# Optimization experiments

Measured on AMD Instinct MI355X. Metric: run time of the kernel, lower is better.

The kernel has to match this reference:

```python
import jax, jax.numpy as jnp
import numpy as np
from jax import lax

BN_EPS = 1e-5

def _bn(x, g, b):
    # eval-mode BatchNorm with default running stats (mean=0, var=1)
    sh = (1, -1) + (1,) * (x.ndim - 2)
    return x * (g / jnp.sqrt(1.0 + BN_EPS)).reshape(sh) + b.reshape(sh)

def _simam(x, lam=1e-4):
    axes = tuple(range(2, x.ndim))
    mu = x.mean(axis=axes, keepdims=True)
    d2 = (x - mu) ** 2
    var = d2.mean(axis=axes, keepdims=True)
    e = d2 / (2.0 * var + 1e-12) + lam
    return jax.nn.sigmoid(1.0 / (e + 1e-12)) * x

def _dwconv1d(x, w, pad, groups):
    return lax.conv_general_dilated(
        x, w, (1,), [(pad, pad)],
        dimension_numbers=('NCH', 'OIH', 'NCH'),
        feature_group_count=groups)

def _adaptive_pool_matrix(t_in, t_out):
    # torch AdaptiveAvgPool1d: window i = [floor(i*t_in/t_out), ceil((i+1)*t_in/t_out))
    M = np.zeros((t_in, t_out), dtype=np.float32)
    for i in range(t_out):
        s = (i * t_in) // t_out
        e = -(-((i + 1) * t_in) // t_out)
        M[s:e, i] = 1.0 / (e - s)
    return jnp.asarray(M)

def _deform_conv1d(x, w, ow, ob):
    # depthwise deformable conv1d, padding='valid'; grid_sample bilinear,
    # zeros padding, align_corners=True -> pure 1D bilinear gather at pos.
    B, C, T = x.shape
    K = w.shape[1]
    T_out = T - K + 1
    off = _dwconv1d(x, ow, 0, C) + ob[None, :, None]        # (B, C*K, T_out)
    off = off.reshape(B, C, K, T_out)
    pos = (jnp.arange(T_out, dtype=x.dtype)[None, None, None, :]
           + jnp.arange(K, dtype=x.dtype)[None, None, :, None] + off)
    i0f = jnp.floor(pos)
    f = pos - i0f
    i0 = i0f.astype(jnp.int32)
    xb = jnp.broadcast_to(x[:, :, None, :], (B, C, K, T))
    def gather(idx):
        valid = (idx >= 0) & (idx < T)
        v = jnp.take_along_axis(xb, jnp.clip(idx, 0, T - 1), axis=3)
        return jnp.where(valid, v, 0.0)
    samp = gather(i0) * (1.0 - f) + gather(i0 + 1) * f      # (B,C,K,T_out)
    return jnp.einsum('bckt,ck->bct', samp, w)

def _branch(x, sw, g1, b1, tw, g2, b2):
    # spatial depthwise conv (kernel covers full channel axis) -> (B,5,T)
    h = jnp.einsum('bcht,ch->bct', x, sw)
    h = _simam(jax.nn.elu(_bn(h, g1, b1)))
    h = _dwconv1d(h, tw, tw.shape[-1] // 2, h.shape[1])     # temporal depthwise, same length
    return _simam(jax.nn.elu(_bn(h, g2, b2)))

def setup_inputs() -> dict:
    key = jax.random.key(0)
    ks = iter(jax.random.split(key, 48))
    B, C_in, T, n_class = 256, 22, 1000, 4
    k1, k2, k3 = 15, 31, 63  # _odd(round(fs*{0.06,0.12,0.25})), fs=250
    def rn(shape, scale=0.1):
        return scale * jax.random.normal(next(ks), shape, dtype=jnp.float32)
    inp = {'x': jax.random.normal(next(ks), (B, 1, C_in, T), dtype=jnp.float32),
           'stem_w': rn((15, 1, 2, 3)),
           'stem_g': 1.0 + rn((15,)), 'stem_b': rn((15,))}
    for i, kt in zip((1, 2, 3), (k1, k2, k3)):
        inp[f'b{i}_sw'] = rn((5, C_in))
        inp[f'b{i}_g1'] = 1.0 + rn((5,)); inp[f'b{i}_b1'] = rn((5,))
        inp[f'b{i}_tw'] = rn((5, 1, kt))
        inp[f'b{i}_g2'] = 1.0 + rn((5,)); inp[f'b{i}_b2'] = rn((5,))
    inp['pw_w'] = rn((5, 15))
    inp['pw_g'] = 1.0 + rn((5,)); inp['pw_b'] = rn((5,))
    inp['d1_w'] = rn((5, 5));  inp['d1_ow'] = rn((25, 1, 5), 0.02);  inp['d1_ob'] = jnp.zeros((25,), jnp.float32)
    inp['d2_w'] = rn((5, 10)); inp['d2_ow'] = rn((50, 1, 10), 0.02); inp['d2_ob'] = jnp.zeros((50,), jnp.float32)
    inp['fc_w'] = rn((n_class, 5 * 25)); inp['fc_b'] = rn((n_class,))
    return inp

def reference(x, stem_w, stem_g, stem_b,
              b1_sw, b1_g1, b1_b1, b1_tw, b1_g2, b1_b2,
              b2_sw, b2_g1, b2_b1, b2_tw, b2_g2, b2_b2,
              b3_sw, b3_g1, b3_b1, b3_tw, b3_g2, b3_b2,
              pw_w, pw_g, pw_b,
              d1_w, d1_ow, d1_ob, d2_w, d2_ow, d2_ob,
              fc_w, fc_b):
    # stem: conv2d k=(2,3) 'same' (torch pads extra on the right for even k)
    h = lax.conv_general_dilated(x, stem_w, (1, 1), [(0, 1), (1, 1)],
                                 dimension_numbers=('NCHW', 'OIHW', 'NCHW'))
    h = jax.nn.elu(_bn(h, stem_g, stem_b))                  # (B,15,22,T); dropout = eval no-op
    o1 = _branch(h[:, 0:5],  b1_sw, b1_g1, b1_b1, b1_tw, b1_g2, b1_b2)
    o2 = _branch(h[:, 5:10], b2_sw, b2_g1, b2_b1, b2_tw, b2_g2, b2_b2)
    o3 = _branch(h[:, 10:15], b3_sw, b3_g1, b3_b1, b3_tw, b3_g2, b3_b2)
    hc = jnp.concatenate([o1, o2, o3], axis=1)              # (B,15,T)
    hc = jnp.einsum('bct,to->bco', hc, _adaptive_pool_matrix(hc.shape[-1], 40))
    hc = jnp.einsum('bct,oc->bot', hc, pw_w)                # 1x1 pointwise
    hc = _simam(jax.nn.elu(_bn(hc, pw_g, pw_b)))            # (B,5,40)
    hc = _deform_conv1d(hc, d1_w, d1_ow, d1_ob)             # (B,5,36)
    hc = _deform_conv1d(hc, d2_w, d2_ow, d2_ob)             # (B,5,27)
    hc = jnp.einsum('bct,to->bco', hc, _adaptive_pool_matrix(hc.shape[-1], 25))
    return hc.reshape(hc.shape[0], -1) @ fc_w.T + fc_b      # (B,n_class)
```

## Files before the change

kernel.cpp:

```cpp
#include <hip/hip_runtime.h>
#include <math.h>

#define BNS 0.99999500003749972f

__device__ __forceinline__ float eluf(float v) {
    return v > 0.f ? v : (__expf(v) - 1.f);
}
__device__ __forceinline__ float sigmf(float u) {
    return 1.f / (1.f + __expf(-u));
}
__device__ __forceinline__ int zpw(int i) { return i + (i >> 5); }

__device__ __forceinline__ void block_reduce2(float& s1, float& s2, float* red) {
#pragma unroll
    for (int m = 32; m > 0; m >>= 1) {
        s1 += __shfl_xor(s1, m, 64);
        s2 += __shfl_xor(s2, m, 64);
    }
    const int wid = threadIdx.x >> 6, lane = threadIdx.x & 63;
    if (lane == 0) { red[wid * 2] = s1; red[wid * 2 + 1] = s2; }
    __syncthreads();
    s1 = red[0] + red[2] + red[4] + red[6];
    s2 = red[1] + red[3] + red[5] + red[7];
}

__global__ __launch_bounds__(256) void k_stem_reg(
    const float* __restrict__ x,
    const float* __restrict__ stem_w,
    const float* __restrict__ stem_g, const float* __restrict__ stem_b,
    const float* __restrict__ sw1, const float* __restrict__ sw2, const float* __restrict__ sw3,
    float* __restrict__ pre)
{
    const int tid = threadIdx.x;
    if (tid >= 250) return;
    const int b = blockIdx.z;
    const int g = blockIdx.y;
    const int t0 = (blockIdx.x * 250 + tid) * 2;
    const float* xb = x + b * 22000;

    const float* swp = (g == 0 ? sw1 : g == 1 ? sw2 : sw3);
    float w[5][6], gs[5], bs[5];
#pragma unroll
    for (int c = 0; c < 5; ++c) {
        const int C = g * 5 + c;
#pragma unroll
        for (int j = 0; j < 6; ++j) w[c][j] = stem_w[C * 6 + j];
        gs[c] = stem_g[C] * BNS;
        bs[c] = stem_b[C];
    }

    const bool sel0 = (t0 == 0), sel2 = (t0 == 998);
    const int base = sel0 ? 0 : (sel2 ? 996 : t0 - 1);

    float acc0[5] = {0, 0, 0, 0, 0}, acc1[5] = {0, 0, 0, 0, 0};

    float a0, b0, c0, d0, a1, b1, c1, d1;
    {
        const float4 v = *reinterpret_cast<const float4*>(xb + base);
        a0 = sel2 ? v.y : (sel0 ? 0.f : v.x);
        b0 = sel0 ? v.x : (sel2 ? v.z : v.y);
        c0 = sel0 ? v.y : (sel2 ? v.w : v.z);
        d0 = sel0 ? v.z : (sel2 ? 0.f : v.w);
    }
#pragma unroll
    for (int i = 0; i < 22; ++i) {
        if (i < 21) {
            const float4 v = *reinterpret_cast<const float4*>(xb + (i + 1) * 1000 + base);
            a1 = sel2 ? v.y : (sel0 ? 0.f : v.x);
            b1 = sel0 ? v.x : (sel2 ? v.z : v.y);
            c1 = sel0 ? v.y : (sel2 ? v.w : v.z);
            d1 = sel0 ? v.z : (sel2 ? 0.f : v.w);
        } else {
            a1 = b1 = c1 = d1 = 0.f;
        }
#pragma unroll
        for (int c = 0; c < 5; ++c) {
            float v0 = w[c][0] * a0 + w[c][1] * b0 + w[c][2] * c0
                     + w[c][3] * a1 + w[c][4] * b1 + w[c][5] * c1;
            float v1 = w[c][0] * b0 + w[c][1] * c0 + w[c][2] * d0
                     + w[c][3] * b1 + w[c][4] * c1 + w[c][5] * d1;
            v0 = eluf(v0 * gs[c] + bs[c]);
            v1 = eluf(v1 * gs[c] + bs[c]);
            const float sv = swp[c * 22 + i];
            acc0[c] += v0 * sv;
            acc1[c] += v1 * sv;
        }
        a0 = a1; b0 = b1; c0 = c1; d0 = d1;
    }
#pragma unroll
    for (int c = 0; c < 5; ++c) {
        float2 o; o.x = acc0[c]; o.y = acc1[c];
        *reinterpret_cast<float2*>(pre + (b * 15 + g * 5 + c) * 1000 + t0) = o;
    }
}

#define PAD 32

template<int K>
__device__ __forceinline__ void branch_body(
    const float* __restrict__ row,
    float g1s, float b1v,
    const float* __restrict__ twp,
    float g2s, float b2v,
    float* __restrict__ out40,
    float* zbuf, float* red)
{
    const int tid = threadIdx.x;
    const int t0 = tid * 4;
    const bool act = tid < 250;

    if (tid < 32) { zbuf[zpw(tid)] = 0.f; zbuf[zpw(1032 + tid)] = 0.f; }

    float y0 = 0.f, y1 = 0.f, y2 = 0.f, y3 = 0.f, s1 = 0.f, s2 = 0.f;
    if (act) {
        const float4 v = *reinterpret_cast<const float4*>(row + t0);
        y0 = eluf(v.x * g1s + b1v);
        y1 = eluf(v.y * g1s + b1v);
        y2 = eluf(v.z * g1s + b1v);
        y3 = eluf(v.w * g1s + b1v);
        s1 = y0 + y1 + y2 + y3;
        s2 = y0 * y0 + y1 * y1 + y2 * y2 + y3 * y3;
    }
    block_reduce2(s1, s2, red);
    {
        const float mu = s1 * 1e-3f;
        const float var = s2 * 1e-3f - mu * mu;
        const float iv = 1.f / (2.f * var + 1e-12f);
        if (act) {
            float d;
            d = y0 - mu; zbuf[zpw(PAD + t0 + 0)] = sigmf(1.f / (d * d * iv + 1e-4f + 1e-12f)) * y0;
            d = y1 - mu; zbuf[zpw(PAD + t0 + 1)] = sigmf(1.f / (d * d * iv + 1e-4f + 1e-12f)) * y1;
            d = y2 - mu; zbuf[zpw(PAD + t0 + 2)] = sigmf(1.f / (d * d * iv + 1e-4f + 1e-12f)) * y2;
            d = y3 - mu; zbuf[zpw(PAD + t0 + 3)] = sigmf(1.f / (d * d * iv + 1e-4f + 1e-12f)) * y3;
        }
    }
    __syncthreads();

    float u0 = 0.f, u1 = 0.f, u2 = 0.f, u3 = 0.f;
    s1 = 0.f; s2 = 0.f;
    if (act) {
        const int Lb = PAD + t0 - (K / 2);
        float q0 = zbuf[zpw(Lb + 0)];
        float q1 = zbuf[zpw(Lb + 1)];
        float q2 = zbuf[zpw(Lb + 2)];
        float q3 = zbuf[zpw(Lb + 3)];
        float a0 = 0.f, a1 = 0.f, a2 = 0.f, a3 = 0.f;
#pragma unroll
        for (int d = 0; d < K; ++d) {
            const float wv = twp[d];
            a0 += q0 * wv; a1 += q1 * wv; a2 += q2 * wv; a3 += q3 * wv;
            q0 = q1; q1 = q2; q2 = q3;
            q3 = zbuf[zpw(Lb + d + 4)];
        }
        u0 = eluf(a0 * g2s + b2v);
        u1 = eluf(a1 * g2s + b2v);
        u2 = eluf(a2 * g2s + b2v);
        u3 = eluf(a3 * g2s + b2v);
        s1 = u0 + u1 + u2 + u3;
        s2 = u0 * u0 + u1 * u1 + u2 * u2 + u3 * u3;
    }
    block_reduce2(s1, s2, red);
    {
        const float mu = s1 * 1e-3f;
        const float var = s2 * 1e-3f - mu * mu;
        const float iv = 1.f / (2.f * var + 1e-12f);
        if (act) {
            float d;
            d = u0 - mu; zbuf[zpw(PAD + t0 + 0)] = sigmf(1.f / (d * d * iv + 1e-4f + 1e-12f)) * u0;
            d = u1 - mu; zbuf[zpw(PAD + t0 + 1)] = sigmf(1.f / (d * d * iv + 1e-4f + 1e-12f)) * u1;
            d = u2 - mu; zbuf[zpw(PAD + t0 + 2)] = sigmf(1.f / (d * d * iv + 1e-4f + 1e-12f)) * u2;
            d = u3 - mu; zbuf[zpw(PAD + t0 + 3)] = sigmf(1.f / (d * d * iv + 1e-4f + 1e-12f)) * u3;
        }
    }
    __syncthreads();

    if (tid < 40) {
        float s = 0.f;
        for (int j = 0; j < 25; ++j) s += zbuf[zpw(PAD + tid * 25 + j)];
        out40[tid] = s * (1.f / 25.f);
    }
}

__global__ __launch_bounds__(256) void k_branch_row(
    const float* __restrict__ pre,
    const float* __restrict__ g1a, const float* __restrict__ b1a,
    const float* __restrict__ tw1,
    const float* __restrict__ g2a, const float* __restrict__ b2a,
    const float* __restrict__ g1b, const float* __restrict__ b1b,
    const float* __restrict__ tw2,
    const float* __restrict__ g2b, const float* __restrict__ b2b,
    const float* __restrict__ g1c, const float* __restrict__ b1c,
    const float* __restrict__ tw3,
    const float* __restrict__ g2c, const float* __restrict__ b2c,
    float* __restrict__ pooled)
{
    __shared__ float zbuf[1100];
    __shared__ float red[8];

    const int bid = blockIdx.x;
    const int b = bid / 15, C = bid % 15;
    const int br = C / 5, c = C % 5;

    const float* row = pre + (b * 15 + C) * 1000;
    float* out40 = pooled + (b * 15 + C) * 40;

    if (br == 0) {
        branch_body<15>(row, g1a[c] * BNS, b1a[c], tw1 + c * 15, g2a[c] * BNS, b2a[c], out40, zbuf, red);
    } else if (br == 1) {
        branch_body<31>(row, g1b[c] * BNS, b1b[c], tw2 + c * 31, g2b[c] * BNS, b2b[c], out40, zbuf, red);
    } else {
        branch_body<63>(row, g1c[c] * BNS, b1c[c], tw3 + c * 63, g2c[c] * BNS, b2c[c], out40, zbuf, red);
    }
}

__global__ __launch_bounds__(128) void k_head(
    const float* __restrict__ pooled,
    const float* __restrict__ pw_w, const float* __restrict__ pw_g, const float* __restrict__ pw_b,
    const float* __restrict__ d1_w, const float* __restrict__ d1_ow, const float* __restrict__ d1_ob,
    const float* __restrict__ d2_w, const float* __restrict__ d2_ow, const float* __restrict__ d2_ob,
    const float* __restrict__ fc_w, const float* __restrict__ fc_b,
    float* __restrict__ out)
{
    __shared__ float P[600];
    __shared__ float A[200];
    __shared__ float Bv[200];
    __shared__ float C1[180];
    __shared__ float C2[135];
    __shared__ float D[125];
    __shared__ float mu5[5], iv5[5];

    const int b = blockIdx.x, tid = threadIdx.x;

    for (int i = tid; i < 600; i += 128) P[i] = pooled[b * 600 + i];
    __syncthreads();

    for (int i = tid; i < 200; i += 128) {
        int o = i / 40, t = i % 40;
        float s = 0.f;
        for (int cc = 0; cc < 15; ++cc) s += P[cc * 40 + t] * pw_w[o * 15 + cc];
        float v = s * (pw_g[o] * BNS) + pw_b[o];
        A[i] = eluf(v);
    }
    __syncthreads();

    if (tid < 5) {
        float s = 0.f;
        for (int t = 0; t < 40; ++t) s += A[tid * 40 + t];
        float mu = s * (1.f / 40.f);
        float v2 = 0.f;
        for (int t = 0; t < 40; ++t) { float d = A[tid * 40 + t] - mu; v2 += d * d; }
        mu5[tid] = mu;
        iv5[tid] = 1.f / (2.f * (v2 * (1.f / 40.f)) + 1e-12f);
    }
    __syncthreads();

    for (int i = tid; i < 200; i += 128) {
        int o = i / 40;
        float a = A[i];
        float d = a - mu5[o];
        float e = d * d * iv5[o] + 1e-4f;
        Bv[i] = sigmf(1.f / (e + 1e-12f)) * a;
    }
    __syncthreads();

    for (int i = tid; i < 180; i += 128) {
        int cc = i / 36, t = i % 36;
        float o = 0.f;
        for (int k = 0; k < 5; ++k) {
            float off = d1_ob[cc * 5 + k];
            for (int d = 0; d < 5; ++d) off += Bv[cc * 40 + t + d] * d1_ow[(cc * 5 + k) * 5 + d];
            float pos = (float)(t + k) + off;
            float fl = floorf(pos);
            float f = pos - fl;
            int i0 = (int)fl;
            float v0 = (i0 >= 0 && i0 < 40) ? Bv[cc * 40 + i0] : 0.f;
            float v1 = (i0 + 1 >= 0 && i0 + 1 < 40) ? Bv[cc * 40 + i0 + 1] : 0.f;
            o += (v0 * (1.f - f) + v1 * f) * d1_w[cc * 5 + k];
        }
        C1[i] = o;
    }
    __syncthreads();

    for (int i = tid; i < 135; i += 128) {
        int cc = i / 27, t = i % 27;
        float o = 0.f;
        for (int k = 0; k < 10; ++k) {
            float off = d2_ob[cc * 10 + k];
            for (int d = 0; d < 10; ++d) off += C1[cc * 36 + t + d] * d2_ow[(cc * 10 + k) * 10 + d];
            float pos = (float)(t + k) + off;
            float fl = floorf(pos);
            float f = pos - fl;
            int i0 = (int)fl;
            float v0 = (i0 >= 0 && i0 < 36) ? C1[cc * 36 + i0] : 0.f;
            float v1 = (i0 + 1 >= 0 && i0 + 1 < 36) ? C1[cc * 36 + i0 + 1] : 0.f;
            o += (v0 * (1.f - f) + v1 * f) * d2_w[cc * 10 + k];
        }
        C2[i] = o;
    }
    __syncthreads();

    for (int i = tid; i < 125; i += 128) {
        int cc = i / 25, j = i % 25;
        int s0 = (j * 27) / 25;
        int e0 = ((j + 1) * 27 + 24) / 25;
        float s = 0.f;
        for (int q = s0; q < e0; ++q) s += C2[cc * 27 + q];
        D[i] = s / (float)(e0 - s0);
    }
    __syncthreads();

    if (tid < 64) {
        float part0 = 0.f, part1 = 0.f, part2 = 0.f, part3 = 0.f;
        for (int i = tid; i < 125; i += 64) {
            const float dv = D[i];
            part0 += dv * fc_w[0 * 125 + i];
            part1 += dv * fc_w[1 * 125 + i];
            part2 += dv * fc_w[2 * 125 + i];
            part3 += dv * fc_w[3 * 125 + i];
        }
#pragma unroll
        for (int m = 32; m > 0; m >>= 1) {
            part0 += __shfl_xor(part0, m, 64);
            part1 += __shfl_xor(part1, m, 64);
            part2 += __shfl_xor(part2, m, 64);
            part3 += __shfl_xor(part3, m, 64);
        }
        if (tid == 0) {
            out[b * 4 + 0] = part0 + fc_b[0];
            out[b * 4 + 1] = part1 + fc_b[1];
            out[b * 4 + 2] = part2 + fc_b[2];
            out[b * 4 + 3] = part3 + fc_b[3];
        }
    }
}

extern "C" void kernel_launch(void* const* d_in, const int* in_sizes, int n_in,
                              void* d_out, int out_size, void* d_ws, size_t ws_size,
                              hipStream_t stream) {
    const float* x      = (const float*)d_in[0];
    const float* stem_w = (const float*)d_in[1];
    const float* stem_g = (const float*)d_in[2];
    const float* stem_b = (const float*)d_in[3];
    const float* b1_sw = (const float*)d_in[4];
    const float* b1_g1 = (const float*)d_in[5];
    const float* b1_b1 = (const float*)d_in[6];
    const float* b1_tw = (const float*)d_in[7];
    const float* b1_g2 = (const float*)d_in[8];
    const float* b1_b2 = (const float*)d_in[9];
    const float* b2_sw = (const float*)d_in[10];
    const float* b2_g1 = (const float*)d_in[11];
    const float* b2_b1 = (const float*)d_in[12];
    const float* b2_tw = (const float*)d_in[13];
    const float* b2_g2 = (const float*)d_in[14];
    const float* b2_b2 = (const float*)d_in[15];
    const float* b3_sw = (const float*)d_in[16];
    const float* b3_g1 = (const float*)d_in[17];
    const float* b3_b1 = (const float*)d_in[18];
    const float* b3_tw = (const float*)d_in[19];
    const float* b3_g2 = (const float*)d_in[20];
    const float* b3_b2 = (const float*)d_in[21];
    const float* pw_w  = (const float*)d_in[22];
    const float* pw_g  = (const float*)d_in[23];
    const float* pw_b  = (const float*)d_in[24];
    const float* d1_w  = (const float*)d_in[25];
    const float* d1_ow = (const float*)d_in[26];
    const float* d1_ob = (const float*)d_in[27];
    const float* d2_w  = (const float*)d_in[28];
    const float* d2_ow = (const float*)d_in[29];
    const float* d2_ob = (const float*)d_in[30];
    const float* fc_w  = (const float*)d_in[31];
    const float* fc_b  = (const float*)d_in[32];

    float* pre    = (float*)d_ws;
    float* pooled = (float*)((char*)d_ws + (size_t)256 * 15 * 1000 * 4);

    k_stem_reg<<<dim3(2, 3, 256), 256, 0, stream>>>(
        x, stem_w, stem_g, stem_b, b1_sw, b2_sw, b3_sw, pre);

    k_branch_row<<<3840, 256, 0, stream>>>(
        pre,
        b1_g1, b1_b1, b1_tw, b1_g2, b1_b2,
        b2_g1, b2_b1, b2_tw, b2_g2, b2_b2,
        b3_g1, b3_b1, b3_tw, b3_g2, b3_b2,
        pooled);

    k_head<<<256, 128, 0, stream>>>(
        pooled, pw_w, pw_g, pw_b,
        d1_w, d1_ow, d1_ob, d2_w, d2_ow, d2_ob,
        fc_w, fc_b, (float*)d_out);
}
```

Baseline: 78.62 us.

## Fuse stem conv and branch kernels, one wavefront per channel row in LDS

Merges the stem/spatial-conv kernel and the per-row branch kernel into one kernel with one block per (batch, branch group). The stem result is kept in LDS instead of a global intermediate, and each of the five channel rows is then handled by a single 64-lane wavefront using shuffle-only reductions with no block barriers. This removes the global round trip of the pre-activation tensor and one launch. In exchange each thread holds 16 outputs plus a sliding window in registers, and only 768 blocks are launched, so occupancy and parallelism drop.

```diff
diff --git a/kernel.cpp b/kernel.cpp
--- a/kernel.cpp
+++ b/kernel.cpp
@@ -11,178 +11,105 @@
 }
 __device__ __forceinline__ int zpw(int i) { return i + (i >> 5); }
 
-__device__ __forceinline__ void block_reduce2(float& s1, float& s2, float* red) {
-#pragma unroll
-    for (int m = 32; m > 0; m >>= 1) {
-        s1 += __shfl_xor(s1, m, 64);
-        s2 += __shfl_xor(s2, m, 64);
-    }
-    const int wid = threadIdx.x >> 6, lane = threadIdx.x & 63;
-    if (lane == 0) { red[wid * 2] = s1; red[wid * 2 + 1] = s2; }
-    __syncthreads();
-    s1 = red[0] + red[2] + red[4] + red[6];
-    s2 = red[1] + red[3] + red[5] + red[7];
-}
-
-__global__ __launch_bounds__(256) void k_stem_reg(
+#define PROW 1032
+#define ZROW 1120
+#define PADZ 32
+
+
+template<int K>
+__device__ __forceinline__ void branch_wave(
+    const float* __restrict__ prow,
+    float g1s, float b1v,
+    const float* __restrict__ twp,
+    float g2s, float b2v,
+    float* __restrict__ zrow,
+    float* __restrict__ out40)
+{
+    const int lane = threadIdx.x & 63;
+    const int tb = lane * 16;
+
+    if (lane < 32) { zrow[zpw(lane)] = 0.f; zrow[zpw(1032 + lane)] = 0.f; }
+
+    float y[16];
+    float s1 = 0.f, s2 = 0.f;
+#pragma unroll
+    for (int j = 0; j < 16; ++j) {
+        const int t = tb + j;
+        float v = 0.f;
+        if (t < 1000) v = eluf(prow[zpw(t)] * g1s + b1v);
+        y[j] = v; s1 += v; s2 += v * v;
+    }
+#pragma unroll
+    for (int m = 32; m > 0; m >>= 1) { s1 += __shfl_xor(s1, m, 64); s2 += __shfl_xor(s2, m, 64); }
+    {
+        const float mu = s1 * 1e-3f;
+        const float var = s2 * 1e-3f - mu * mu;
+        const float iv = 1.f / (2.f * var + 1e-12f);
+#pragma unroll
+        for (int j = 0; j < 16; ++j) {
+            const int t = tb + j;
+            if (t < 1000) {
+                const float d = y[j] - mu;
+                zrow[zpw(PADZ + t)] = sigmf(1.f / (d * d * iv + 1e-4f + 1e-12f)) * y[j];
+            }
+        }
+    }
+
+    const int Lb = PADZ + tb - (K / 2);
+    float win[16];
+#pragma unroll
+    for (int j = 0; j < 15; ++j) win[j] = zrow[zpw(Lb + j)];
+    float a[16];
+#pragma unroll
+    for (int j = 0; j < 16; ++j) a[j] = 0.f;
+#pragma unroll
+    for (int d = 0; d < K; ++d) {
+        win[15] = zrow[zpw(Lb + d + 15)];
+        const float wv = twp[d];
+#pragma unroll
+        for (int j = 0; j < 16; ++j) a[j] += win[j] * wv;
+#pragma unroll
+        for (int j = 0; j < 15; ++j) win[j] = win[j + 1];
+    }
+
+    float u[16];
+    s1 = 0.f; s2 = 0.f;
+#pragma unroll
+    for (int j = 0; j < 16; ++j) {
+        const int t = tb + j;
+        float v = 0.f;
+        if (t < 1000) v = eluf(a[j] * g2s + b2v);
+        u[j] = v; s1 += v; s2 += v * v;
+    }
+#pragma unroll
+    for (int m = 32; m > 0; m >>= 1) { s1 += __shfl_xor(s1, m, 64); s2 += __shfl_xor(s2, m, 64); }
+    {
+        const float mu = s1 * 1e-3f;
+        const float var = s2 * 1e-3f - mu * mu;
+        const float iv = 1.f / (2.f * var + 1e-12f);
+#pragma unroll
+        for (int j = 0; j < 16; ++j) {
+            const int t = tb + j;
+            if (t < 1000) {
+                const float d = u[j] - mu;
+                zrow[zpw(PADZ + t)] = sigmf(1.f / (d * d * iv + 1e-4f + 1e-12f)) * u[j];
+            }
+        }
+    }
+
+    if (lane < 40) {
+        float s = 0.f;
+#pragma unroll
+        for (int q = 0; q < 25; ++q) s += zrow[zpw(PADZ + lane * 25 + q)];
+        out40[lane] = s * (1.f / 25.f);
+    }
+}
+
+__global__ __launch_bounds__(320) void k_fused(
     const float* __restrict__ x,
     const float* __restrict__ stem_w,
     const float* __restrict__ stem_g, const float* __restrict__ stem_b,
     const float* __restrict__ sw1, const float* __restrict__ sw2, const float* __restrict__ sw3,
-    float* __restrict__ pre)
-{
-    const int tid = threadIdx.x;
-    if (tid >= 250) return;
-    const int b = blockIdx.z;
-    const int g = blockIdx.y;
-    const int t0 = (blockIdx.x * 250 + tid) * 2;
-    const float* xb = x + b * 22000;
-
-    const float* swp = (g == 0 ? sw1 : g == 1 ? sw2 : sw3);
-    float w[5][6], gs[5], bs[5];
-#pragma unroll
-    for (int c = 0; c < 5; ++c) {
-        const int C = g * 5 + c;
-#pragma unroll
-        for (int j = 0; j < 6; ++j) w[c][j] = stem_w[C * 6 + j];
-        gs[c] = stem_g[C] * BNS;
-        bs[c] = stem_b[C];
-    }
-
-    const bool sel0 = (t0 == 0), sel2 = (t0 == 998);
-    const int base = sel0 ? 0 : (sel2 ? 996 : t0 - 1);
-
-    float acc0[5] = {0, 0, 0, 0, 0}, acc1[5] = {0, 0, 0, 0, 0};
-
-    float a0, b0, c0, d0, a1, b1, c1, d1;
-    {
-        const float4 v = *reinterpret_cast<const float4*>(xb + base);
-        a0 = sel2 ? v.y : (sel0 ? 0.f : v.x);
-        b0 = sel0 ? v.x : (sel2 ? v.z : v.y);
-        c0 = sel0 ? v.y : (sel2 ? v.w : v.z);
-        d0 = sel0 ? v.z : (sel2 ? 0.f : v.w);
-    }
-#pragma unroll
-    for (int i = 0; i < 22; ++i) {
-        if (i < 21) {
-            const float4 v = *reinterpret_cast<const float4*>(xb + (i + 1) * 1000 + base);
-            a1 = sel2 ? v.y : (sel0 ? 0.f : v.x);
-            b1 = sel0 ? v.x : (sel2 ? v.z : v.y);
-            c1 = sel0 ? v.y : (sel2 ? v.w : v.z);
-            d1 = sel0 ? v.z : (sel2 ? 0.f : v.w);
-        } else {
-            a1 = b1 = c1 = d1 = 0.f;
-        }
-#pragma unroll
-        for (int c = 0; c < 5; ++c) {
-            float v0 = w[c][0] * a0 + w[c][1] * b0 + w[c][2] * c0
-                     + w[c][3] * a1 + w[c][4] * b1 + w[c][5] * c1;
-            float v1 = w[c][0] * b0 + w[c][1] * c0 + w[c][2] * d0
-                     + w[c][3] * b1 + w[c][4] * c1 + w[c][5] * d1;
-            v0 = eluf(v0 * gs[c] + bs[c]);
-            v1 = eluf(v1 * gs[c] + bs[c]);
-            const float sv = swp[c * 22 + i];
-            acc0[c] += v0 * sv;
-            acc1[c] += v1 * sv;
-        }
-        a0 = a1; b0 = b1; c0 = c1; d0 = d1;
-    }
-#pragma unroll
-    for (int c = 0; c < 5; ++c) {
-        float2 o; o.x = acc0[c]; o.y = acc1[c];
-        *reinterpret_cast<float2*>(pre + (b * 15 + g * 5 + c) * 1000 + t0) = o;
-    }
-}
-
-#define PAD 32
-
-template<int K>
-__device__ __forceinline__ void branch_body(
-    const float* __restrict__ row,
-    float g1s, float b1v,
-    const float* __restrict__ twp,
-    float g2s, float b2v,
-    float* __restrict__ out40,
-    float* zbuf, float* red)
-{
-    const int tid = threadIdx.x;
-    const int t0 = tid * 4;
-    const bool act = tid < 250;
-
-    if (tid < 32) { zbuf[zpw(tid)] = 0.f; zbuf[zpw(1032 + tid)] = 0.f; }
-
-    float y0 = 0.f, y1 = 0.f, y2 = 0.f, y3 = 0.f, s1 = 0.f, s2 = 0.f;
-    if (act) {
-        const float4 v = *reinterpret_cast<const float4*>(row + t0);
-        y0 = eluf(v.x * g1s + b1v);
-        y1 = eluf(v.y * g1s + b1v);
-        y2 = eluf(v.z * g1s + b1v);
-        y3 = eluf(v.w * g1s + b1v);
-        s1 = y0 + y1 + y2 + y3;
-        s2 = y0 * y0 + y1 * y1 + y2 * y2 + y3 * y3;
-    }
-    block_reduce2(s1, s2, red);
-    {
-        const float mu = s1 * 1e-3f;
-        const float var = s2 * 1e-3f - mu * mu;
-        const float iv = 1.f / (2.f * var + 1e-12f);
-        if (act) {
-            float d;
-            d = y0 - mu; zbuf[zpw(PAD + t0 + 0)] = sigmf(1.f / (d * d * iv + 1e-4f + 1e-12f)) * y0;
-            d = y1 - mu; zbuf[zpw(PAD + t0 + 1)] = sigmf(1.f / (d * d * iv + 1e-4f + 1e-12f)) * y1;
-            d = y2 - mu; zbuf[zpw(PAD + t0 + 2)] = sigmf(1.f / (d * d * iv + 1e-4f + 1e-12f)) * y2;
-            d = y3 - mu; zbuf[zpw(PAD + t0 + 3)] = sigmf(1.f / (d * d * iv + 1e-4f + 1e-12f)) * y3;
-        }
-    }
-    __syncthreads();
-
-    float u0 = 0.f, u1 = 0.f, u2 = 0.f, u3 = 0.f;
-    s1 = 0.f; s2 = 0.f;
-    if (act) {
-        const int Lb = PAD + t0 - (K / 2);
-        float q0 = zbuf[zpw(Lb + 0)];
-        float q1 = zbuf[zpw(Lb + 1)];
-        float q2 = zbuf[zpw(Lb + 2)];
-        float q3 = zbuf[zpw(Lb + 3)];
-        float a0 = 0.f, a1 = 0.f, a2 = 0.f, a3 = 0.f;
-#pragma unroll
-        for (int d = 0; d < K; ++d) {
-            const float wv = twp[d];
-            a0 += q0 * wv; a1 += q1 * wv; a2 += q2 * wv; a3 += q3 * wv;
-            q0 = q1; q1 = q2; q2 = q3;
-            q3 = zbuf[zpw(Lb + d + 4)];
-        }
-        u0 = eluf(a0 * g2s + b2v);
-        u1 = eluf(a1 * g2s + b2v);
-        u2 = eluf(a2 * g2s + b2v);
-        u3 = eluf(a3 * g2s + b2v);
-        s1 = u0 + u1 + u2 + u3;
-        s2 = u0 * u0 + u1 * u1 + u2 * u2 + u3 * u3;
-    }
-    block_reduce2(s1, s2, red);
-    {
-        const float mu = s1 * 1e-3f;
-        const float var = s2 * 1e-3f - mu * mu;
-        const float iv = 1.f / (2.f * var + 1e-12f);
-        if (act) {
-            float d;
-            d = u0 - mu; zbuf[zpw(PAD + t0 + 0)] = sigmf(1.f / (d * d * iv + 1e-4f + 1e-12f)) * u0;
-            d = u1 - mu; zbuf[zpw(PAD + t0 + 1)] = sigmf(1.f / (d * d * iv + 1e-4f + 1e-12f)) * u1;
-            d = u2 - mu; zbuf[zpw(PAD + t0 + 2)] = sigmf(1.f / (d * d * iv + 1e-4f + 1e-12f)) * u2;
-            d = u3 - mu; zbuf[zpw(PAD + t0 + 3)] = sigmf(1.f / (d * d * iv + 1e-4f + 1e-12f)) * u3;
-        }
-    }
-    __syncthreads();
-
-    if (tid < 40) {
-        float s = 0.f;
-        for (int j = 0; j < 25; ++j) s += zbuf[zpw(PAD + tid * 25 + j)];
-        out40[tid] = s * (1.f / 25.f);
-    }
-}
-
-__global__ __launch_bounds__(256) void k_branch_row(
-    const float* __restrict__ pre,
     const float* __restrict__ g1a, const float* __restrict__ b1a,
     const float* __restrict__ tw1,
     const float* __restrict__ g2a, const float* __restrict__ b2a,
@@ -194,22 +121,99 @@
     const float* __restrict__ g2c, const float* __restrict__ b2c,
     float* __restrict__ pooled)
 {
-    __shared__ float zbuf[1100];
-    __shared__ float red[8];
-
+    __shared__ float preL[5 * PROW];
+    __shared__ float zsh[5 * ZROW];
+
+    const int tid = threadIdx.x;
     const int bid = blockIdx.x;
-    const int b = bid / 15, C = bid % 15;
-    const int br = C / 5, c = C % 5;
-
-    const float* row = pre + (b * 15 + C) * 1000;
-    float* out40 = pooled + (b * 15 + C) * 40;
-
-    if (br == 0) {
-        branch_body<15>(row, g1a[c] * BNS, b1a[c], tw1 + c * 15, g2a[c] * BNS, b2a[c], out40, zbuf, red);
-    } else if (br == 1) {
-        branch_body<31>(row, g1b[c] * BNS, b1b[c], tw2 + c * 31, g2b[c] * BNS, b2b[c], out40, zbuf, red);
+    const int b = bid / 3, g = bid % 3;
+    const float* xb = x + b * 22000;
+
+    if (tid < 250) {
+        const int t0 = tid * 4;
+        const int mode = (tid == 0) ? 0 : (tid == 249 ? 2 : 1);
+        const float* swp = (g == 0 ? sw1 : g == 1 ? sw2 : sw3);
+
+        float wv[5][6], gs[5], bsv[5];
+#pragma unroll
+        for (int c = 0; c < 5; ++c) {
+            const int C = g * 5 + c;
+#pragma unroll
+            for (int j = 0; j < 6; ++j) wv[c][j] = stem_w[C * 6 + j];
+            gs[c] = stem_g[C] * BNS;
+            bsv[c] = stem_b[C];
+        }
+
+        float acc[5][4];
+#pragma unroll
+        for (int c = 0; c < 5; ++c)
+#pragma unroll
+            for (int j = 0; j < 4; ++j) acc[c][j] = 0.f;
+
+        float cw[6], nw[6];
+        #define LOADROW(r, w6)                                                        \
+        {                                                                             \
+            const float* rp = xb + (r) * 1000;                                        \
+            if (mode == 1) {                                                          \
+                const float4 v4 = *reinterpret_cast<const float4*>(rp + t0 - 1);      \
+                const float2 v2 = *reinterpret_cast<const float2*>(rp + t0 + 3);      \
+                w6[0] = v4.x; w6[1] = v4.y; w6[2] = v4.z; w6[3] = v4.w;               \
+                w6[4] = v2.x; w6[5] = v2.y;                                           \
+            } else if (mode == 0) {                                                   \
+                const float4 v4 = *reinterpret_cast<const float4*>(rp);               \
+                w6[0] = 0.f; w6[1] = v4.x; w6[2] = v4.y; w6[3] = v4.z;                \
+                w6[4] = v4.w; w6[5] = rp[4];                                          \
+            } else {                                                                  \
+                const float4 v4 = *reinterpret_cast<const float4*>(rp + 995);         \
+                w6[0] = v4.x; w6[1] = v4.y; w6[2] = v4.z; w6[3] = v4.w;               \
+                w6[4] = rp[999]; w6[5] = 0.f;                                         \
+            }                                                                         \
+        }
+
+        LOADROW(0, cw)
+#pragma unroll
+        for (int i = 0; i < 22; ++i) {
+            if (i < 21) {
+                LOADROW(i + 1, nw)
+            } else {
+#pragma unroll
+                for (int j = 0; j < 6; ++j) nw[j] = 0.f;
+            }
+#pragma unroll
+            for (int c = 0; c < 5; ++c) {
+                const float sv = swp[c * 22 + i];
+#pragma unroll
+                for (int j = 0; j < 4; ++j) {
+                    float v = wv[c][0] * cw[j] + wv[c][1] * cw[j + 1] + wv[c][2] * cw[j + 2]
+                            + wv[c][3] * nw[j] + wv[c][4] * nw[j + 1] + wv[c][5] * nw[j + 2];
+                    v = eluf(v * gs[c] + bsv[c]);
+                    acc[c][j] += v * sv;
+                }
+            }
+#pragma unroll
+            for (int j = 0; j < 6; ++j) cw[j] = nw[j];
+        }
+        #undef LOADROW
+
+#pragma unroll
+        for (int c = 0; c < 5; ++c)
+#pragma unroll
+            for (int j = 0; j < 4; ++j)
+                preL[c * PROW + zpw(t0 + j)] = acc[c][j];
+    }
+    __syncthreads();
+
+    const int w = tid >> 6;
+    float* zrow = zsh + w * ZROW;
+    const float* prow = preL + w * PROW;
+    float* out40 = pooled + (b * 15 + g * 5 + w) * 40;
+
+    if (g == 0) {
+        branch_wave<15>(prow, g1a[w] * BNS, b1a[w], tw1 + w * 15, g2a[w] * BNS, b2a[w], zrow, out40);
+    } else if (g == 1) {
+        branch_wave<31>(prow, g1b[w] * BNS, b1b[w], tw2 + w * 31, g2b[w] * BNS, b2b[w], zrow, out40);
     } else {
-        branch_body<63>(row, g1c[c] * BNS, b1c[c], tw3 + c * 63, g2c[c] * BNS, b2c[c], out40, zbuf, red);
+        branch_wave<63>(prow, g1c[w] * BNS, b1c[w], tw3 + w * 63, g2c[w] * BNS, b2c[w], zrow, out40);
     }
 }
 
@@ -371,14 +375,10 @@
     const float* fc_w  = (const float*)d_in[31];
     const float* fc_b  = (const float*)d_in[32];
 
-    float* pre    = (float*)d_ws;
-    float* pooled = (float*)((char*)d_ws + (size_t)256 * 15 * 1000 * 4);
-
-    k_stem_reg<<<dim3(2, 3, 256), 256, 0, stream>>>(
-        x, stem_w, stem_g, stem_b, b1_sw, b2_sw, b3_sw, pre);
-
-    k_branch_row<<<3840, 256, 0, stream>>>(
-        pre,
+    float* pooled = (float*)d_ws;
+
+    k_fused<<<768, 320, 0, stream>>>(
+        x, stem_w, stem_g, stem_b, b1_sw, b2_sw, b3_sw,
         b1_g1, b1_b1, b1_tw, b1_g2, b1_b2,
         b2_g1, b2_b1, b2_tw, b2_g2, b2_b2,
         b3_g1, b3_b1, b3_tw, b3_g2, b3_b2,
```

Result: slower. 111.2 us (+41.5%).
